# Kernel optimization log

Hardware: AMD Instinct MI355X
Metric: run time of the kernel (lower is better)

## Reference

```python
import jax, jax.numpy as jnp
import numpy as np

C1 = 0.01 ** 2
C2 = 0.03 ** 2
EPS = 1e-8


def _box3(t):
    # 3x3 mean filter, zero padding (SAME), NCHW, 1 channel.
    k = jnp.full((1, 1, 3, 3), 1.0 / 9.0, dtype=t.dtype)
    return jax.lax.conv_general_dilated(
        t, k, window_strides=(1, 1), padding=((1, 1), (1, 1)),
        dimension_numbers=("NCHW", "OIHW", "NCHW"))


def setup_inputs() -> dict:
    key = jax.random.key(0)
    k1, k2 = jax.random.split(key)
    shape = (32, 1, 1024, 1024)
    x = jax.random.uniform(k1, shape, dtype=jnp.float32)
    y = jax.random.uniform(k2, shape, dtype=jnp.float32)
    return {"x": x, "y": y}


def reference(x, y):
    mu_x = _box3(x)
    mu_y = _box3(y)
    sigma_x = _box3(x * x) - mu_x * mu_x
    sigma_y = _box3(y * y) - mu_y * mu_y
    sigma_xy = _box3(x * y) - mu_x * mu_y
    ssim_map = ((2.0 * mu_x * mu_y + C1) * (2.0 * sigma_xy + C2)
                / ((mu_x ** 2 + mu_y ** 2 + C1) * (sigma_x + sigma_y + C2) + EPS))
    return 1.0 - jnp.mean(ssim_map)
```

## Files before the change

kernel.cpp:

```cpp
#include <hip/hip_runtime.h>

#define IMG_H 1024
#define IMG_W 1024
#define RPB   32
#define TPB   256

__device__ __forceinline__ void hsum_row(const float* __restrict__ xr,
                                         const float* __restrict__ yr,
                                         int c,
                                         float* hx, float* hy,
                                         float* hxx, float* hyy, float* hxy)
{
    float4 xv = *reinterpret_cast<const float4*>(xr + c);
    float4 yv = *reinterpret_cast<const float4*>(yr + c);
    float xs[6], ys[6];
    xs[0] = (c > 0) ? xr[c - 1] : 0.0f;
    ys[0] = (c > 0) ? yr[c - 1] : 0.0f;
    xs[1] = xv.x; xs[2] = xv.y; xs[3] = xv.z; xs[4] = xv.w;
    ys[1] = yv.x; ys[2] = yv.y; ys[3] = yv.z; ys[4] = yv.w;
    xs[5] = (c + 4 < IMG_W) ? xr[c + 4] : 0.0f;
    ys[5] = (c + 4 < IMG_W) ? yr[c + 4] : 0.0f;

    float pxx[6], pyy[6], pxy[6];
#pragma unroll
    for (int k = 0; k < 6; ++k) {
        pxx[k] = xs[k] * xs[k];
        pyy[k] = ys[k] * ys[k];
        pxy[k] = xs[k] * ys[k];
    }
#pragma unroll
    for (int j = 0; j < 4; ++j) {
        hx[j]  = xs[j]  + xs[j + 1]  + xs[j + 2];
        hy[j]  = ys[j]  + ys[j + 1]  + ys[j + 2];
        hxx[j] = pxx[j] + pxx[j + 1] + pxx[j + 2];
        hyy[j] = pyy[j] + pyy[j + 1] + pyy[j + 2];
        hxy[j] = pxy[j] + pxy[j + 1] + pxy[j + 2];
    }
}

__global__ __launch_bounds__(TPB)
void ssim_map_sum_kernel(const float* __restrict__ x,
                         const float* __restrict__ y,
                         float* __restrict__ ws_sum)
{
    const int rb = blockIdx.x;
    const int n  = blockIdx.y;
    const int r0 = rb * RPB;
    const int c  = (int)threadIdx.x * 4;

    const float* xi = x + (size_t)n * IMG_H * IMG_W;
    const float* yi = y + (size_t)n * IMG_H * IMG_W;

    const float C1   = 0.01f * 0.01f;
    const float C2   = 0.03f * 0.03f;
    const float EPSv = 1e-8f;
    const float inv9 = 1.0f / 9.0f;

    float hAx[4], hAy[4], hAxx[4], hAyy[4], hAxy[4];
    float hBx[4], hBy[4], hBxx[4], hByy[4], hBxy[4];
    float hCx[4], hCy[4], hCxx[4], hCyy[4], hCxy[4];

    if (r0 > 0) {
        hsum_row(xi + (size_t)(r0 - 1) * IMG_W, yi + (size_t)(r0 - 1) * IMG_W,
                 c, hAx, hAy, hAxx, hAyy, hAxy);
    } else {
#pragma unroll
        for (int j = 0; j < 4; ++j) { hAx[j]=0.f; hAy[j]=0.f; hAxx[j]=0.f; hAyy[j]=0.f; hAxy[j]=0.f; }
    }
    hsum_row(xi + (size_t)r0 * IMG_W, yi + (size_t)r0 * IMG_W,
             c, hBx, hBy, hBxx, hByy, hBxy);

    float acc = 0.0f;

    for (int i = 0; i < RPB; ++i) {
        const int r = r0 + i;
        if (r + 1 < IMG_H) {
            hsum_row(xi + (size_t)(r + 1) * IMG_W, yi + (size_t)(r + 1) * IMG_W,
                     c, hCx, hCy, hCxx, hCyy, hCxy);
        } else {
#pragma unroll
            for (int j = 0; j < 4; ++j) { hCx[j]=0.f; hCy[j]=0.f; hCxx[j]=0.f; hCyy[j]=0.f; hCxy[j]=0.f; }
        }

#pragma unroll
        for (int j = 0; j < 4; ++j) {
            const float sx  = hAx[j]  + hBx[j]  + hCx[j];
            const float sy  = hAy[j]  + hBy[j]  + hCy[j];
            const float sxx = hAxx[j] + hBxx[j] + hCxx[j];
            const float syy = hAyy[j] + hByy[j] + hCyy[j];
            const float sxy = hAxy[j] + hBxy[j] + hCxy[j];

            const float mu_x = sx * inv9;
            const float mu_y = sy * inv9;
            const float mxx  = mu_x * mu_x;
            const float myy  = mu_y * mu_y;
            const float mxy  = mu_x * mu_y;
            const float sigx  = sxx * inv9 - mxx;
            const float sigy  = syy * inv9 - myy;
            const float sigxy = sxy * inv9 - mxy;

            const float num = (2.0f * mxy + C1) * (2.0f * sigxy + C2);
            const float den = (mxx + myy + C1) * (sigx + sigy + C2) + EPSv;
            acc += num / den;
        }

#pragma unroll
        for (int j = 0; j < 4; ++j) {
            hAx[j]=hBx[j]; hAy[j]=hBy[j]; hAxx[j]=hBxx[j]; hAyy[j]=hByy[j]; hAxy[j]=hBxy[j];
            hBx[j]=hCx[j]; hBy[j]=hCy[j]; hBxx[j]=hCxx[j]; hByy[j]=hCyy[j]; hBxy[j]=hCxy[j];
        }
    }

#pragma unroll
    for (int off = 32; off > 0; off >>= 1)
        acc += __shfl_down(acc, off);

    __shared__ float red[TPB / 64];
    const int lane = (int)threadIdx.x & 63;
    const int wave = (int)threadIdx.x >> 6;
    if (lane == 0) red[wave] = acc;
    __syncthreads();
    if (threadIdx.x == 0) {
        float s = 0.0f;
#pragma unroll
        for (int w = 0; w < TPB / 64; ++w) s += red[w];
        atomicAdd(ws_sum, s);
    }
}

__global__ void ssim_finalize_kernel(const float* __restrict__ ws_sum,
                                     float* __restrict__ out,
                                     float inv_count)
{
    out[0] = 1.0f - ws_sum[0] * inv_count;
}

extern "C" void kernel_launch(void* const* d_in, const int* in_sizes, int n_in,
                              void* d_out, int out_size, void* d_ws, size_t ws_size,
                              hipStream_t stream)
{
    const float* x = (const float*)d_in[0];
    const float* y = (const float*)d_in[1];
    float* out  = (float*)d_out;
    float* wsum = (float*)d_ws;

    const long long total = (long long)in_sizes[0];
    const int N = (int)(total / ((long long)IMG_H * IMG_W));

    hipMemsetAsync(wsum, 0, sizeof(float), stream);

    dim3 grid(IMG_H / RPB, N);
    ssim_map_sum_kernel<<<grid, TPB, 0, stream>>>(x, y, wsum);

    ssim_finalize_kernel<<<1, 1, 0, stream>>>(wsum, out, 1.0f / (float)total);
}
```

Measured before the change: 292.4 us.

## Rescale SSIM algebra, use fast reciprocal, fully unroll rotating row buffers

```diff
diff --git a/kernel.cpp b/kernel.cpp
--- a/kernel.cpp
+++ b/kernel.cpp
@@ -2,14 +2,20 @@
 
 #define IMG_H 1024
 #define IMG_W 1024
-#define RPB   32
+#define RPB   16
 #define TPB   256
 
-__device__ __forceinline__ void hsum_row(const float* __restrict__ xr,
-                                         const float* __restrict__ yr,
-                                         int c,
-                                         float* hx, float* hy,
-                                         float* hxx, float* hyy, float* hxy)
+struct HS { float x[4], y[4], xx[4], yy[4], xy[4]; };
+
+__device__ __forceinline__ void zero_hs(HS& h)
+{
+#pragma unroll
+    for (int j = 0; j < 4; ++j) { h.x[j]=0.f; h.y[j]=0.f; h.xx[j]=0.f; h.yy[j]=0.f; h.xy[j]=0.f; }
+}
+
+__device__ __forceinline__ void load_hs(const float* __restrict__ xr,
+                                        const float* __restrict__ yr,
+                                        int c, HS& h)
 {
     float4 xv = *reinterpret_cast<const float4*>(xr + c);
     float4 yv = *reinterpret_cast<const float4*>(yr + c);
@@ -30,11 +36,37 @@
     }
 #pragma unroll
     for (int j = 0; j < 4; ++j) {
-        hx[j]  = xs[j]  + xs[j + 1]  + xs[j + 2];
-        hy[j]  = ys[j]  + ys[j + 1]  + ys[j + 2];
-        hxx[j] = pxx[j] + pxx[j + 1] + pxx[j + 2];
-        hyy[j] = pyy[j] + pyy[j + 1] + pyy[j + 2];
-        hxy[j] = pxy[j] + pxy[j + 1] + pxy[j + 2];
+        h.x[j]  = xs[j]  + xs[j + 1]  + xs[j + 2];
+        h.y[j]  = ys[j]  + ys[j + 1]  + ys[j + 2];
+        h.xx[j] = pxx[j] + pxx[j + 1] + pxx[j + 2];
+        h.yy[j] = pyy[j] + pyy[j + 1] + pyy[j + 2];
+        h.xy[j] = pxy[j] + pxy[j + 1] + pxy[j + 2];
+    }
+}
+
+__device__ __forceinline__ void accum(const HS& A, const HS& B, const HS& C, float& acc)
+{
+    const float c1s  = 81.0f * 1e-4f;
+    const float c2s  = 81.0f * 9e-4f;
+    const float epss = 6561.0f * 1e-8f;
+#pragma unroll
+    for (int j = 0; j < 4; ++j) {
+        const float sx  = A.x[j]  + B.x[j]  + C.x[j];
+        const float sy  = A.y[j]  + B.y[j]  + C.y[j];
+        const float sxx = A.xx[j] + B.xx[j] + C.xx[j];
+        const float syy = A.yy[j] + B.yy[j] + C.yy[j];
+        const float sxy = A.xy[j] + B.xy[j] + C.xy[j];
+
+        const float t1 = sx * sy;
+        const float t2 = fmaf(sx, sx, sy * sy);
+        const float s2 = sxx + syy;
+        const float An = fmaf(2.0f, t1, c1s);
+        const float Bn = fmaf(-2.0f, t1, fmaf(18.0f, sxy, c2s));
+        const float Xd = t2 + c1s;
+        const float Yd = fmaf(9.0f, s2, c2s - t2);
+        const float den = fmaf(Xd, Yd, epss);
+        const float num = An * Bn;
+        acc = fmaf(num, __builtin_amdgcn_rcpf(den), acc);
     }
 }
 
@@ -51,65 +83,30 @@
     const float* xi = x + (size_t)n * IMG_H * IMG_W;
     const float* yi = y + (size_t)n * IMG_H * IMG_W;
 
-    const float C1   = 0.01f * 0.01f;
-    const float C2   = 0.03f * 0.03f;
-    const float EPSv = 1e-8f;
-    const float inv9 = 1.0f / 9.0f;
-
-    float hAx[4], hAy[4], hAxx[4], hAyy[4], hAxy[4];
-    float hBx[4], hBy[4], hBxx[4], hByy[4], hBxy[4];
-    float hCx[4], hCy[4], hCxx[4], hCyy[4], hCxy[4];
-
-    if (r0 > 0) {
-        hsum_row(xi + (size_t)(r0 - 1) * IMG_W, yi + (size_t)(r0 - 1) * IMG_W,
-                 c, hAx, hAy, hAxx, hAyy, hAxy);
-    } else {
-#pragma unroll
-        for (int j = 0; j < 4; ++j) { hAx[j]=0.f; hAy[j]=0.f; hAxx[j]=0.f; hAyy[j]=0.f; hAxy[j]=0.f; }
-    }
-    hsum_row(xi + (size_t)r0 * IMG_W, yi + (size_t)r0 * IMG_W,
-             c, hBx, hBy, hBxx, hByy, hBxy);
+    HS hA, hB, hC;
+    if (r0 > 0) load_hs(xi + (size_t)(r0 - 1) * IMG_W, yi + (size_t)(r0 - 1) * IMG_W, c, hA);
+    else        zero_hs(hA);
+    load_hs(xi + (size_t)r0 * IMG_W, yi + (size_t)r0 * IMG_W, c, hB);
 
     float acc = 0.0f;
 
-    for (int i = 0; i < RPB; ++i) {
-        const int r = r0 + i;
-        if (r + 1 < IMG_H) {
-            hsum_row(xi + (size_t)(r + 1) * IMG_W, yi + (size_t)(r + 1) * IMG_W,
-                     c, hCx, hCy, hCxx, hCyy, hCxy);
-        } else {
-#pragma unroll
-            for (int j = 0; j < 4; ++j) { hCx[j]=0.f; hCy[j]=0.f; hCxx[j]=0.f; hCyy[j]=0.f; hCxy[j]=0.f; }
-        }
+#define STEP(P, Q, R, k)                                                          \
+    {                                                                             \
+        const int nr = r0 + (k) + 1;                                              \
+        if (nr < IMG_H)                                                           \
+            load_hs(xi + (size_t)nr * IMG_W, yi + (size_t)nr * IMG_W, c, R);      \
+        else                                                                      \
+            zero_hs(R);                                                           \
+        accum(P, Q, R, acc);                                                      \
+    }
 
-#pragma unroll
-        for (int j = 0; j < 4; ++j) {
-            const float sx  = hAx[j]  + hBx[j]  + hCx[j];
-            const float sy  = hAy[j]  + hBy[j]  + hCy[j];
-            const float sxx = hAxx[j] + hBxx[j] + hCxx[j];
-            const float syy = hAyy[j] + hByy[j] + hCyy[j];
-            const float sxy = hAxy[j] + hBxy[j] + hCxy[j];
-
-            const float mu_x = sx * inv9;
-            const float mu_y = sy * inv9;
-            const float mxx  = mu_x * mu_x;
-            const float myy  = mu_y * mu_y;
-            const float mxy  = mu_x * mu_y;
-            const float sigx  = sxx * inv9 - mxx;
-            const float sigy  = syy * inv9 - myy;
-            const float sigxy = sxy * inv9 - mxy;
-
-            const float num = (2.0f * mxy + C1) * (2.0f * sigxy + C2);
-            const float den = (mxx + myy + C1) * (sigx + sigy + C2) + EPSv;
-            acc += num / den;
-        }
-
-#pragma unroll
-        for (int j = 0; j < 4; ++j) {
-            hAx[j]=hBx[j]; hAy[j]=hBy[j]; hAxx[j]=hBxx[j]; hAyy[j]=hByy[j]; hAxy[j]=hBxy[j];
-            hBx[j]=hCx[j]; hBy[j]=hCy[j]; hBxx[j]=hCxx[j]; hByy[j]=hCyy[j]; hBxy[j]=hCxy[j];
-        }
-    }
+    STEP(hA, hB, hC, 0)   STEP(hB, hC, hA, 1)   STEP(hC, hA, hB, 2)
+    STEP(hA, hB, hC, 3)   STEP(hB, hC, hA, 4)   STEP(hC, hA, hB, 5)
+    STEP(hA, hB, hC, 6)   STEP(hB, hC, hA, 7)   STEP(hC, hA, hB, 8)
+    STEP(hA, hB, hC, 9)   STEP(hB, hC, hA, 10)  STEP(hC, hA, hB, 11)
+    STEP(hA, hB, hC, 12)  STEP(hB, hC, hA, 13)  STEP(hC, hA, hB, 14)
+    STEP(hA, hB, hC, 15)
+#undef STEP
 
 #pragma unroll
     for (int off = 32; off > 0; off >>= 1)
```

Result: slower. 359.4 us (+22.9%).
